# Kernel tuning notes

Measured on AMD Instinct MI355X. Metric: run time of the kernel, lower is better.

## Reference

```python
import jax, jax.numpy as jnp
from jax import lax
import numpy as np

B, D, T = 4096, 64, 8
H, K, NC = 128, 32, 10


def setup_inputs() -> dict:
    key = jax.random.key(0)
    ks = jax.random.split(key, 16)
    def w(k, shape, fan_in):
        return (jax.random.normal(k, shape) / np.float32(np.sqrt(fan_in))).astype(jnp.float32)
    return {
        "x": jax.random.normal(ks[0], (B, D, T), jnp.float32),
        "sx": jnp.zeros((B, H), jnp.float32),
        "Wih": w(ks[1], (3 * H, D), D),
        "Whh": w(ks[2], (3 * H, H), H),
        "bih": w(ks[3], (3 * H,), H),
        "bhh": w(ks[4], (3 * H,), H),
        "We": w(ks[5], (2 * K, H), H),
        "be": w(ks[6], (2 * K,), H),
        "Wl": w(ks[7], (H, K), K),
        "bl": w(ks[8], (H,), K),
        "Wo": w(ks[9], (NC, H), H),
        "bo": w(ks[10], (NC,), H),
        "Whalt": w(ks[11], (1, H), H),
        "bhalt": w(ks[12], (1,), H),
        "M": 14,
    }


def _gru_cell(x, h, Wih, Whh, bih, bhh):
    gi = x @ Wih.T + bih  # [B, 3H]
    gh = h @ Whh.T + bhh  # [B, 3H]
    i_r, i_z, i_n = jnp.split(gi, 3, axis=1)
    h_r, h_z, h_n = jnp.split(gh, 3, axis=1)
    r = jax.nn.sigmoid(i_r + h_r)
    zg = jax.nn.sigmoid(i_z + h_z)
    n = jnp.tanh(i_n + r * h_n)
    return (1.0 - zg) * n + zg * h


def reference(x, sx, Wih, Whh, bih, bhh, We, be, Wl, bl, Wo, bo, Whalt, bhalt, M):
    # step_type='act' (the default). We run the full M ticks (no early break);
    # since ph weights past the halting point are zero, yt/st/pt/nt match.
    Tn = x.shape[-1]
    keys = jax.random.split(jax.random.key(42), Tn * M).reshape(Tn, M)
    xT = jnp.moveaxis(x, -1, 0)  # [T, B, D]

    def act_step(h_carry, inp):
        xi, ks = inp  # xi [B, D], ks [M] keys

        def tick(h_state, k):
            h = _gru_cell(xi, h_state, Wih, Whh, bih, bhh)
            enc = h @ We.T + be                    # [B, 2K]
            mus = enc[:, :K]
            sigmas = jax.nn.softplus(enc[:, K:] - 5.0)
            z = jax.random.normal(k, sigmas.shape, sigmas.dtype) * sigmas + mus
            hb = jnp.tanh(z @ Wl.T + bl)           # bottleneck -> hidden
            y = hb @ Wo.T + bo                     # [B, NC]
            pn = jax.nn.sigmoid(hb @ Whalt.T + bhalt)[:, 0]  # [B]
            return hb, (pn, y, hb)

        _, (p_hist, y_hist, s_hist) = lax.scan(tick, h_carry, ks)
        p_hist = p_hist.T                          # [B, M]
        p_max = jnp.minimum(1.0, jnp.cumsum(p_hist, axis=1))
        p_max = p_max.at[:, -1].set(1.0)
        ph = jnp.concatenate([p_max[:, :1], jnp.diff(p_max, axis=1)], axis=1)  # [B, M]
        st = jnp.einsum('bm,mbh->bh', ph, s_hist)  # ACT-weighted state
        yt = jnp.einsum('bm,mbc->bc', ph, y_hist)  # ACT-weighted output
        nt = jnp.argmax(p_max, axis=1)             # first tick reaching max
        rt = 1.0 - jnp.take_along_axis(p_max, ((nt - 1) % M)[:, None], axis=1)[:, 0]
        pt = nt.astype(yt.dtype) + rt              # ponder cost
        return st, (yt, pt, nt)

    sx_final, (Y, P, N) = lax.scan(act_step, sx, (xT, keys))
    # Y: [T,B,NC] -> [B,NC,T]; P: [T,B] -> [B,T]; N: [T,B] -> [B,T]
    return jnp.moveaxis(Y, 0, -1), P.T, N.T, sx_final
```

## Files before the change

### kernel.cpp

```cpp
#include <hip/hip_runtime.h>
#include <hip/hip_bf16.h>
#include <stdint.h>

#define B_ 4096
#define D_ 64
#define T_ 8
#define H_ 128
#define K_ 32
#define NC_ 10
#define M_ 14

#define P_OFF (B_*NC_*T_)
#define N_OFF (P_OFF + B_*T_)
#define SX_OFF (N_OFF + B_*T_)

#define ROWS 8
#define THREADS 512

#define WS_WHH 0
#define WS_WIH 49152
#define WS_WE  73728
#define WS_WL  81920
#define WS_TOT 86016

__device__ __forceinline__ void tf2x32(uint32_t k0, uint32_t k1,
                                       uint32_t c0, uint32_t c1,
                                       uint32_t& o0, uint32_t& o1) {
  uint32_t ks2 = k0 ^ k1 ^ 0x1BD11BDAu;
  uint32_t x0 = c0 + k0, x1 = c1 + k1;
#define TF_R(r) { x0 += x1; x1 = ((x1 << (r)) | (x1 >> (32 - (r)))); x1 ^= x0; }
  TF_R(13) TF_R(15) TF_R(26) TF_R(6)
  x0 += k1; x1 += ks2 + 1u;
  TF_R(17) TF_R(29) TF_R(16) TF_R(24)
  x0 += ks2; x1 += k0 + 2u;
  TF_R(13) TF_R(15) TF_R(26) TF_R(6)
  x0 += k0; x1 += k1 + 3u;
  TF_R(17) TF_R(29) TF_R(16) TF_R(24)
  x0 += k1; x1 += ks2 + 4u;
  TF_R(13) TF_R(15) TF_R(26) TF_R(6)
  x0 += ks2; x1 += k0 + 5u;
#undef TF_R
  o0 = x0; o1 = x1;
}

__device__ __forceinline__ float erfinv_f(float x) {
  float w = -log1pf(-x * x);
  float p;
  if (w < 5.0f) {
    w -= 2.5f;
    p = 2.81022636e-08f;
    p = fmaf(p, w, 3.43273939e-07f);
    p = fmaf(p, w, -3.5233877e-06f);
    p = fmaf(p, w, -4.39150654e-06f);
    p = fmaf(p, w, 0.00021858087f);
    p = fmaf(p, w, -0.00125372503f);
    p = fmaf(p, w, -0.00417768164f);
    p = fmaf(p, w, 0.246640727f);
    p = fmaf(p, w, 1.50140941f);
  } else {
    w = sqrtf(w) - 3.0f;
    p = -0.000200214257f;
    p = fmaf(p, w, 0.000100950558f);
    p = fmaf(p, w, 0.00134934322f);
    p = fmaf(p, w, -0.00367342844f);
    p = fmaf(p, w, 0.00573950773f);
    p = fmaf(p, w, -0.0076224613f);
    p = fmaf(p, w, 0.00943887047f);
    p = fmaf(p, w, 1.00167406f);
    p = fmaf(p, w, 2.83297682f);
  }
  return p * x;
}

__device__ __forceinline__ float sigmoid_f(float x) { return 1.0f / (1.0f + expf(-x)); }
__device__ __forceinline__ float softplus_f(float x) {
  return (x > 0.0f) ? (x + log1pf(expf(-x))) : log1pf(expf(x));
}

__launch_bounds__(256)
__global__ void reorder_kernel(const float* __restrict__ Whh, const float* __restrict__ Wih,
                               const float* __restrict__ We, const float* __restrict__ Wl,
                               float* __restrict__ ws) {
  int i = (int)blockIdx.x * 256 + (int)threadIdx.x;
  if (i < 49152) {
    int e = i & 3, ch = i >> 2, j = ch % 384, kk = ch / 384;
    ws[WS_WHH + i] = Whh[j * H_ + kk * 4 + e];
  } else if (i < 73728) {
    int x2 = i - WS_WIH;
    int e = x2 & 3, ch = x2 >> 2, j = ch % 384, kk = ch / 384;
    ws[i] = Wih[j * D_ + kk * 4 + e];
  } else if (i < 81920) {
    int x2 = i - WS_WE;
    int e = x2 & 3, ch = x2 >> 2, j = ch % 64, kk = ch / 64;
    ws[i] = We[j * H_ + kk * 4 + e];
  } else if (i < WS_TOT) {
    int x2 = i - WS_WL;
    int e = x2 & 3, ch = x2 >> 2, j = ch % 128, kk = ch / 128;
    ws[i] = Wl[j * K_ + kk * 4 + e];
  }
}

__launch_bounds__(THREADS, 2)
__global__ void vrnn_kernel(const float* __restrict__ x, const float* __restrict__ sx,
                            const float* __restrict__ bih, const float* __restrict__ bhh,
                            const float* __restrict__ be, const float* __restrict__ bl,
                            const float* __restrict__ Wo, const float* __restrict__ bo,
                            const float* __restrict__ Whalt, const float* __restrict__ bhalt,
                            const float* __restrict__ ws, float* __restrict__ out) {
  __shared__ float sh_hA[ROWS][132];
  __shared__ float sh_hB[ROWS][132];
  __shared__ float sh_gh[384 * 9];
  __shared__ float sh_gi[384 * 9];
  __shared__ float sh_z[ROWS][36];
  __shared__ float sh_x[ROWS][68];
  __shared__ uint32_t sh_keys[T_ * M_][2];

  const int tid = (int)threadIdx.x;
  const int r = tid & 7;
  const int idx = tid >> 3;
  const int i0 = idx * 2;
  const int c = idx >> 2;
  const int q = idx & 3;
  const int blk = (int)blockIdx.x;
  const int b = blk * ROWS + r;
  const bool isrow = (tid < 384);

  const float* whh2 = ws + WS_WHH;
  const float* wih2 = ws + WS_WIH;
  const float* we2  = ws + WS_WE;
  const float* wl2  = ws + WS_WL;

  if (tid < T_ * M_) {
    uint32_t o0, o1;
    tf2x32(0u, 42u, 0u, (uint32_t)tid, o0, o1);
    sh_keys[tid][0] = o0;
    sh_keys[tid][1] = o1;
  }

  float bhh_j = 0.0f, bih_j = 0.0f;
  if (isrow) { bhh_j = bhh[tid]; bih_j = bih[tid]; }

#pragma unroll
  for (int e = tid; e < ROWS * H_; e += THREADS)
    sh_hA[e >> 7][e & 127] = sx[blk * ROWS * H_ + e];
  __syncthreads();

#pragma unroll 1
  for (int t = 0; t < T_; ++t) {
    { int row = tid >> 6, d = tid & 63;
      sh_x[row][d] = x[(blk * ROWS + row) * (D_ * T_) + d * T_ + t]; }
    __syncthreads();

    if (isrow) {
      float acc[8];
#pragma unroll
      for (int rr = 0; rr < 8; ++rr) acc[rr] = bih_j;
#pragma unroll 2
      for (int kk = 0; kk < D_ / 4; ++kk) {
        float4 wv = *(const float4*)(wih2 + (kk * 384 + tid) * 4);
#pragma unroll
        for (int rr = 0; rr < 8; ++rr) {
          float4 hv = *(const float4*)&sh_x[rr][kk * 4];
          acc[rr] = fmaf(wv.x, hv.x, acc[rr]);
          acc[rr] = fmaf(wv.y, hv.y, acc[rr]);
          acc[rr] = fmaf(wv.z, hv.z, acc[rr]);
          acc[rr] = fmaf(wv.w, hv.w, acc[rr]);
        }
      }
#pragma unroll
      for (int rr = 0; rr < 8; ++rr) sh_gi[tid * 9 + rr] = acc[rr];
    }

    float st0 = 0.0f, st1 = 0.0f, yt = 0.0f;
    float csum = 0.0f, pmprev = 0.0f, rt = 0.0f;
    int nt = -1;

#pragma unroll 1
    for (int m = 0; m < M_; ++m) {
      if (isrow) {
        float acc[8];
#pragma unroll
        for (int rr = 0; rr < 8; ++rr) acc[rr] = bhh_j;
#pragma unroll 2
        for (int kk = 0; kk < H_ / 4; ++kk) {
          float4 wv = *(const float4*)(whh2 + (kk * 384 + tid) * 4);
#pragma unroll
          for (int rr = 0; rr < 8; ++rr) {
            float4 hv = *(const float4*)&sh_hA[rr][kk * 4];
            acc[rr] = fmaf(wv.x, hv.x, acc[rr]);
            acc[rr] = fmaf(wv.y, hv.y, acc[rr]);
            acc[rr] = fmaf(wv.z, hv.z, acc[rr]);
            acc[rr] = fmaf(wv.w, hv.w, acc[rr]);
          }
        }
#pragma unroll
        for (int rr = 0; rr < 8; ++rr) sh_gh[tid * 9 + rr] = acc[rr];
      }
      __syncthreads();

#pragma unroll
      for (int vv = 0; vv < 2; ++vv) {
        int v = tid + vv * THREADS;
        int rr = v & 7, i = v >> 3;
        float ghr = sh_gh[(0 * H_ + i) * 9 + rr];
        float ghz = sh_gh[(1 * H_ + i) * 9 + rr];
        float ghn = sh_gh[(2 * H_ + i) * 9 + rr];
        float gir = sh_gi[(0 * H_ + i) * 9 + rr];
        float giz = sh_gi[(1 * H_ + i) * 9 + rr];
        float gin = sh_gi[(2 * H_ + i) * 9 + rr];
        float rg = sigmoid_f(gir + ghr);
        float zg = sigmoid_f(giz + ghz);
        float ng = tanhf(fmaf(rg, ghn, gin));
        float hprev = sh_hA[rr][i];
        sh_hB[rr][i] = (1.0f - zg) * ng + zg * hprev;
      }
      __syncthreads();

      {
        int wr = tid & 63, rr2 = tid >> 6;
        float acc = be[wr];
#pragma unroll 4
        for (int kk = 0; kk < H_ / 4; ++kk) {
          float4 wv = *(const float4*)(we2 + (kk * 64 + wr) * 4);
          float4 hv = *(const float4*)&sh_hB[rr2][kk * 4];
          acc = fmaf(wv.x, hv.x, acc);
          acc = fmaf(wv.y, hv.y, acc);
          acc = fmaf(wv.z, hv.z, acc);
          acc = fmaf(wv.w, hv.w, acc);
        }
        float accP = __shfl_xor(acc, 32);
        if (wr < K_) {
          float sg = softplus_f(accP - 5.0f);
          uint32_t key0 = sh_keys[t * M_ + m][0];
          uint32_t key1 = sh_keys[t * M_ + m][1];
          uint32_t e = (uint32_t)(blk * ROWS + rr2) * 32u + (uint32_t)wr;
          uint32_t r0, r1;
          tf2x32(key0, key1, 0u, e, r0, r1);
          uint32_t bits = r0 ^ r1;
          float f = __uint_as_float((bits >> 9) | 0x3f800000u) - 1.0f;
          float u = fmaf(f, 2.0f, -0.99999994f);
          u = fmaxf(-0.99999994f, u);
          float eps = 1.41421356f * erfinv_f(u);
          sh_z[rr2][wr] = fmaf(eps, sg, acc);
        }
      }
      __syncthreads();

      {
        int jl = tid & 127, rh = tid >> 7;
        float a0 = bl[jl], a1 = a0;
#pragma unroll
        for (int kk = 0; kk < K_ / 4; ++kk) {
          float4 wv = *(const float4*)(wl2 + (kk * 128 + jl) * 4);
          float4 z0 = *(const float4*)&sh_z[rh * 2][kk * 4];
          float4 z1 = *(const float4*)&sh_z[rh * 2 + 1][kk * 4];
          a0 = fmaf(wv.x, z0.x, a0); a1 = fmaf(wv.x, z1.x, a1);
          a0 = fmaf(wv.y, z0.y, a0); a1 = fmaf(wv.y, z1.y, a1);
          a0 = fmaf(wv.z, z0.z, a0); a1 = fmaf(wv.z, z1.z, a1);
          a0 = fmaf(wv.w, z0.w, a0); a1 = fmaf(wv.w, z1.w, a1);
        }
        sh_hA[rh * 2][jl] = tanhf(a0);
        sh_hA[rh * 2 + 1][jl] = tanhf(a1);
      }
      __syncthreads();

      {
        float pa = bhalt[0];
#pragma unroll 2
        for (int kk = 0; kk < H_ / 4; ++kk) {
          float4 hv = *(const float4*)&sh_hA[r][kk * 4];
          float4 av = *(const float4*)(Whalt + kk * 4);
          pa = fmaf(av.x, hv.x, pa); pa = fmaf(av.y, hv.y, pa);
          pa = fmaf(av.z, hv.z, pa); pa = fmaf(av.w, hv.w, pa);
        }
        float pn = sigmoid_f(pa);

        float yv = 0.0f;
        if (c < NC_) {
          float yq = (q == 0) ? bo[c] : 0.0f;
          const float* wo = Wo + c * H_ + q * 32;
#pragma unroll
          for (int kk = 0; kk < 8; ++kk) {
            float4 hv = *(const float4*)&sh_hA[r][q * 32 + kk * 4];
            float4 ov = *(const float4*)(wo + kk * 4);
            yq = fmaf(ov.x, hv.x, yq); yq = fmaf(ov.y, hv.y, yq);
            yq = fmaf(ov.z, hv.z, yq); yq = fmaf(ov.w, hv.w, yq);
          }
          yq += __shfl_xor(yq, 8);
          yq += __shfl_xor(yq, 16);
          yv = yq;
        }

        csum += pn;
        float pm = (m == M_ - 1) ? 1.0f : fminf(1.0f, csum);
        if (nt < 0 && (csum >= 1.0f || m == M_ - 1)) {
          nt = m;
          rt = (m == 0) ? 0.0f : (1.0f - pmprev);
        }
        float ph = pm - pmprev;
        pmprev = pm;
        st0 = fmaf(ph, sh_hA[r][i0], st0);
        st1 = fmaf(ph, sh_hA[r][i0 + 1], st1);
        yt = fmaf(ph, yv, yt);
      }

      if (__syncthreads_and(csum >= 1.0f)) break;
    }

    __syncthreads();
    sh_hA[r][i0] = st0;
    sh_hA[r][i0 + 1] = st1;
    if (c < NC_ && q == 0) out[b * (NC_ * T_) + c * T_ + t] = yt;
    if (idx == 40) {
      out[P_OFF + b * T_ + t] = (float)nt + rt;
      out[N_OFF + b * T_ + t] = (float)nt;
    }
    if (t == T_ - 1) {
      out[SX_OFF + b * H_ + i0] = st0;
      out[SX_OFF + b * H_ + i0 + 1] = st1;
    }
    __syncthreads();
  }
}

extern "C" void kernel_launch(void* const* d_in, const int* in_sizes, int n_in,
                              void* d_out, int out_size, void* d_ws, size_t ws_size,
                              hipStream_t stream) {
  (void)in_sizes; (void)n_in; (void)out_size; (void)ws_size;
  const float* x     = (const float*)d_in[0];
  const float* sx    = (const float*)d_in[1];
  const float* Wih   = (const float*)d_in[2];
  const float* Whh   = (const float*)d_in[3];
  const float* bih   = (const float*)d_in[4];
  const float* bhh   = (const float*)d_in[5];
  const float* We    = (const float*)d_in[6];
  const float* be    = (const float*)d_in[7];
  const float* Wl    = (const float*)d_in[8];
  const float* bl    = (const float*)d_in[9];
  const float* Wo    = (const float*)d_in[10];
  const float* bo    = (const float*)d_in[11];
  const float* Whalt = (const float*)d_in[12];
  const float* bhalt = (const float*)d_in[13];
  float* ws  = (float*)d_ws;
  float* out = (float*)d_out;

  reorder_kernel<<<dim3((WS_TOT + 255) / 256), dim3(256), 0, stream>>>(Whh, Wih, We, Wl, ws);
  vrnn_kernel<<<dim3(B_ / ROWS), dim3(THREADS), 0, stream>>>(x, sx, bih, bhh, be, bl,
                                                             Wo, bo, Whalt, bhalt, ws, out);
}
```

Baseline: 657.9 us.

## Use transposed hidden/input layout with packed FMA, compute halt once per row

```diff
diff --git a/kernel.cpp b/kernel.cpp
--- a/kernel.cpp
+++ b/kernel.cpp
@@ -22,6 +22,17 @@
 #define WS_WE  73728
 #define WS_WL  81920
 #define WS_TOT 86016
+
+typedef float v2f __attribute__((ext_vector_type(2)));
+
+#if __has_builtin(__builtin_elementwise_fma)
+#define FMA2(a, b, c) __builtin_elementwise_fma((a), (b), (c))
+#else
+static __device__ __forceinline__ v2f fma2_(v2f a, v2f b, v2f c) {
+  v2f r; r.x = fmaf(a.x, b.x, c.x); r.y = fmaf(a.y, b.y, c.y); return r;
+}
+#define FMA2(a, b, c) fma2_((a), (b), (c))
+#endif
 
 __device__ __forceinline__ void tf2x32(uint32_t k0, uint32_t k1,
                                        uint32_t c0, uint32_t c1,
@@ -108,11 +119,13 @@
                             const float* __restrict__ Whalt, const float* __restrict__ bhalt,
                             const float* __restrict__ ws, float* __restrict__ out) {
   __shared__ float sh_hA[ROWS][132];
+  __shared__ float sh_hAi[H_][12];
   __shared__ float sh_hB[ROWS][132];
   __shared__ float sh_gh[384 * 9];
   __shared__ float sh_gi[384 * 9];
   __shared__ float sh_z[ROWS][36];
-  __shared__ float sh_x[ROWS][68];
+  __shared__ float sh_xi[D_][12];
+  __shared__ float sh_pn[ROWS];
   __shared__ uint32_t sh_keys[T_ * M_][2];
 
   const int tid = (int)threadIdx.x;
@@ -141,34 +154,40 @@
   if (isrow) { bhh_j = bhh[tid]; bih_j = bih[tid]; }
 
 #pragma unroll
-  for (int e = tid; e < ROWS * H_; e += THREADS)
-    sh_hA[e >> 7][e & 127] = sx[blk * ROWS * H_ + e];
+  for (int e = tid; e < ROWS * H_; e += THREADS) {
+    float v = sx[blk * ROWS * H_ + e];
+    sh_hA[e >> 7][e & 127] = v;
+    sh_hAi[e & 127][e >> 7] = v;
+  }
   __syncthreads();
 
 #pragma unroll 1
   for (int t = 0; t < T_; ++t) {
     { int row = tid >> 6, d = tid & 63;
-      sh_x[row][d] = x[(blk * ROWS + row) * (D_ * T_) + d * T_ + t]; }
+      sh_xi[d][row] = x[(blk * ROWS + row) * (D_ * T_) + d * T_ + t]; }
     __syncthreads();
 
     if (isrow) {
-      float acc[8];
-#pragma unroll
-      for (int rr = 0; rr < 8; ++rr) acc[rr] = bih_j;
+      v2f acc[4];
+#pragma unroll
+      for (int p = 0; p < 4; ++p) acc[p] = (v2f){bih_j, bih_j};
 #pragma unroll 2
       for (int kk = 0; kk < D_ / 4; ++kk) {
         float4 wv = *(const float4*)(wih2 + (kk * 384 + tid) * 4);
 #pragma unroll
-        for (int rr = 0; rr < 8; ++rr) {
-          float4 hv = *(const float4*)&sh_x[rr][kk * 4];
-          acc[rr] = fmaf(wv.x, hv.x, acc[rr]);
-          acc[rr] = fmaf(wv.y, hv.y, acc[rr]);
-          acc[rr] = fmaf(wv.z, hv.z, acc[rr]);
-          acc[rr] = fmaf(wv.w, hv.w, acc[rr]);
-        }
-      }
-#pragma unroll
-      for (int rr = 0; rr < 8; ++rr) sh_gi[tid * 9 + rr] = acc[rr];
+        for (int ki = 0; ki < 4; ++ki) {
+          float wsc = (ki == 0) ? wv.x : (ki == 1) ? wv.y : (ki == 2) ? wv.z : wv.w;
+          const v2f* hp = (const v2f*)&sh_xi[kk * 4 + ki][0];
+          v2f wb = (v2f){wsc, wsc};
+#pragma unroll
+          for (int p = 0; p < 4; ++p) acc[p] = FMA2(wb, hp[p], acc[p]);
+        }
+      }
+#pragma unroll
+      for (int p = 0; p < 4; ++p) {
+        sh_gi[tid * 9 + 2 * p]     = acc[p].x;
+        sh_gi[tid * 9 + 2 * p + 1] = acc[p].y;
+      }
     }
 
     float st0 = 0.0f, st1 = 0.0f, yt = 0.0f;
@@ -178,23 +197,26 @@
 #pragma unroll 1
     for (int m = 0; m < M_; ++m) {
       if (isrow) {
-        float acc[8];
-#pragma unroll
-        for (int rr = 0; rr < 8; ++rr) acc[rr] = bhh_j;
+        v2f acc[4];
+#pragma unroll
+        for (int p = 0; p < 4; ++p) acc[p] = (v2f){bhh_j, bhh_j};
 #pragma unroll 2
         for (int kk = 0; kk < H_ / 4; ++kk) {
           float4 wv = *(const float4*)(whh2 + (kk * 384 + tid) * 4);
 #pragma unroll
-          for (int rr = 0; rr < 8; ++rr) {
-            float4 hv = *(const float4*)&sh_hA[rr][kk * 4];
-            acc[rr] = fmaf(wv.x, hv.x, acc[rr]);
-            acc[rr] = fmaf(wv.y, hv.y, acc[rr]);
-            acc[rr] = fmaf(wv.z, hv.z, acc[rr]);
-            acc[rr] = fmaf(wv.w, hv.w, acc[rr]);
+          for (int ki = 0; ki < 4; ++ki) {
+            float wsc = (ki == 0) ? wv.x : (ki == 1) ? wv.y : (ki == 2) ? wv.z : wv.w;
+            const v2f* hp = (const v2f*)&sh_hAi[kk * 4 + ki][0];
+            v2f wb = (v2f){wsc, wsc};
+#pragma unroll
+            for (int p = 0; p < 4; ++p) acc[p] = FMA2(wb, hp[p], acc[p]);
           }
         }
 #pragma unroll
-        for (int rr = 0; rr < 8; ++rr) sh_gh[tid * 9 + rr] = acc[rr];
+        for (int p = 0; p < 4; ++p) {
+          sh_gh[tid * 9 + 2 * p]     = acc[p].x;
+          sh_gh[tid * 9 + 2 * p + 1] = acc[p].y;
+        }
       }
       __syncthreads();
 
@@ -259,12 +281,14 @@
           a0 = fmaf(wv.z, z0.z, a0); a1 = fmaf(wv.z, z1.z, a1);
           a0 = fmaf(wv.w, z0.w, a0); a1 = fmaf(wv.w, z1.w, a1);
         }
-        sh_hA[rh * 2][jl] = tanhf(a0);
-        sh_hA[rh * 2 + 1][jl] = tanhf(a1);
-      }
-      __syncthreads();
-
-      {
+        float t0 = tanhf(a0), t1 = tanhf(a1);
+        sh_hA[rh * 2][jl] = t0;
+        sh_hA[rh * 2 + 1][jl] = t1;
+        *(v2f*)&sh_hAi[jl][rh * 2] = (v2f){t0, t1};
+      }
+      __syncthreads();
+
+      if (idx == 63) {
         float pa = bhalt[0];
 #pragma unroll 2
         for (int kk = 0; kk < H_ / 4; ++kk) {
@@ -273,24 +297,27 @@
           pa = fmaf(av.x, hv.x, pa); pa = fmaf(av.y, hv.y, pa);
           pa = fmaf(av.z, hv.z, pa); pa = fmaf(av.w, hv.w, pa);
         }
-        float pn = sigmoid_f(pa);
-
-        float yv = 0.0f;
-        if (c < NC_) {
-          float yq = (q == 0) ? bo[c] : 0.0f;
-          const float* wo = Wo + c * H_ + q * 32;
-#pragma unroll
-          for (int kk = 0; kk < 8; ++kk) {
-            float4 hv = *(const float4*)&sh_hA[r][q * 32 + kk * 4];
-            float4 ov = *(const float4*)(wo + kk * 4);
-            yq = fmaf(ov.x, hv.x, yq); yq = fmaf(ov.y, hv.y, yq);
-            yq = fmaf(ov.z, hv.z, yq); yq = fmaf(ov.w, hv.w, yq);
-          }
-          yq += __shfl_xor(yq, 8);
-          yq += __shfl_xor(yq, 16);
-          yv = yq;
-        }
-
+        sh_pn[r] = sigmoid_f(pa);
+      }
+      float yv = 0.0f;
+      if (c < NC_) {
+        float yq = (q == 0) ? bo[c] : 0.0f;
+        const float* wo = Wo + c * H_ + q * 32;
+#pragma unroll
+        for (int kk = 0; kk < 8; ++kk) {
+          float4 hv = *(const float4*)&sh_hA[r][q * 32 + kk * 4];
+          float4 ov = *(const float4*)(wo + kk * 4);
+          yq = fmaf(ov.x, hv.x, yq); yq = fmaf(ov.y, hv.y, yq);
+          yq = fmaf(ov.z, hv.z, yq); yq = fmaf(ov.w, hv.w, yq);
+        }
+        yq += __shfl_xor(yq, 8);
+        yq += __shfl_xor(yq, 16);
+        yv = yq;
+      }
+      __syncthreads();
+
+      {
+        float pn = sh_pn[r];
         csum += pn;
         float pm = (m == M_ - 1) ? 1.0f : fminf(1.0f, csum);
         if (nt < 0 && (csum >= 1.0f || m == M_ - 1)) {
@@ -310,6 +337,8 @@
     __syncthreads();
     sh_hA[r][i0] = st0;
     sh_hA[r][i0 + 1] = st1;
+    sh_hAi[i0][r] = st0;
+    sh_hAi[i0 + 1][r] = st1;
     if (c < NC_ && q == 0) out[b * (NC_ * T_) + c * T_ + t] = yt;
     if (idx == 40) {
       out[P_OFF + b * T_ + t] = (float)nt + rt;
```

Measured after the change: 1.004 ms. 1.53x slower.
